# Optimization experiments

Measured on AMD Instinct MI355X. Metric: run time of the kernel, lower is better.

The kernel has to match this reference:

```python
import jax, jax.numpy as jnp
import numpy as np

Q_MAX = 127.0  # symmetric int8 range

def setup_inputs() -> dict:
    key = jax.random.key(0)
    k1, k2, k3, k4 = jax.random.split(key, 4)
    B, S, K, N = 4, 2048, 4096, 4096
    inp = jax.random.normal(k1, (B, S, K), dtype=jnp.float32)
    # int8 weight in [-127, 127], stored via randint(0,255)-127 per spec
    qweight = (jax.random.randint(k2, (N, K), 0, 255) - 127).astype(jnp.int8)
    # per-out-channel weight dequant scales (small positive)
    wparams = (jax.random.uniform(k3, (N,), dtype=jnp.float32) * 0.02 + 0.001)
    bias = jax.random.normal(k4, (N,), dtype=jnp.float32) * 0.1
    return {"inp": inp, "qweight": qweight, "wparams": wparams, "bias": bias}

def reference(inp, qweight, wparams, bias):
    # inp: [B, S, K] float32; qweight: [N, K] int8; wparams: [N]; bias: [N]
    B, S, K = inp.shape
    x = inp.reshape(B * S, K)
    # qntz: per-row symmetric absmax quantization of the activation to int8
    a_scale = jnp.max(jnp.abs(x), axis=1, keepdims=True) / Q_MAX  # [M, 1]
    qinp = jnp.clip(jnp.round(x / a_scale), -Q_MAX, Q_MAX).astype(jnp.int8)  # [M, K]
    d = jax.lax.dot_general(qinp, qweight.T, (((1,), (0,)), ((), ())),
                            preferred_element_type=jnp.int32)  # [M, N]
    # dqntz: scale by per-row act scale and per-col weight scale, add bias
    out = d.astype(jnp.float32) * a_scale * wparams[None, :] + bias[None, :]
    return out.reshape(B, S, -1)
```

## Files before the change

kernel.cpp:

```cpp
#include <hip/hip_runtime.h>
#include <hip/hip_bf16.h>


using int32x4 = __attribute__((ext_vector_type(4))) int;

#define QMAXF 127.0f

__global__ __launch_bounds__(256) void repack_weights(
    const int* __restrict__ w, signed char* __restrict__ w8, int total)
{
    bool is32 = true;
#pragma unroll
    for (int i = 0; i < 16; ++i) {
        int v = w[i];
        is32 = is32 && (v >= -127 && v <= 127);
    }

    const int t = blockIdx.x * blockDim.x + threadIdx.x;
    const int nth = gridDim.x * blockDim.x;
    const int chunks = total / 16;

    if (is32) {
        for (int c = t; c < chunks; c += nth) {
            const int32x4* src = reinterpret_cast<const int32x4*>(w + (size_t)c * 16);
            int32x4 a0 = src[0], a1 = src[1], a2 = src[2], a3 = src[3];
            int32x4 o;
            o[0] = (a0[0] & 0xff) | ((a0[1] & 0xff) << 8) | ((a0[2] & 0xff) << 16) | ((a0[3] & 0xff) << 24);
            o[1] = (a1[0] & 0xff) | ((a1[1] & 0xff) << 8) | ((a1[2] & 0xff) << 16) | ((a1[3] & 0xff) << 24);
            o[2] = (a2[0] & 0xff) | ((a2[1] & 0xff) << 8) | ((a2[2] & 0xff) << 16) | ((a2[3] & 0xff) << 24);
            o[3] = (a3[0] & 0xff) | ((a3[1] & 0xff) << 8) | ((a3[2] & 0xff) << 16) | ((a3[3] & 0xff) << 24);
            reinterpret_cast<int32x4*>(w8)[c] = o;
        }
    } else {
        const int32x4* src = reinterpret_cast<const int32x4*>(w);
        int32x4* dst = reinterpret_cast<int32x4*>(w8);
        for (int c = t; c < chunks; c += nth) dst[c] = src[c];
    }
}

__global__ __launch_bounds__(256) void quant_rows(
    const float* __restrict__ x, signed char* __restrict__ q,
    float* __restrict__ scale, int K)
{
    const int row = blockIdx.x;
    const int t = threadIdx.x;
    const float4* xr = reinterpret_cast<const float4*>(x + (size_t)row * K);

    float4 v[4];
    float m = 0.f;
#pragma unroll
    for (int i = 0; i < 4; ++i) {
        v[i] = xr[t + i * 256];
        m = fmaxf(m, fmaxf(fmaxf(fabsf(v[i].x), fabsf(v[i].y)),
                           fmaxf(fabsf(v[i].z), fabsf(v[i].w))));
    }
#pragma unroll
    for (int off = 32; off >= 1; off >>= 1)
        m = fmaxf(m, __shfl_xor(m, off, 64));
    __shared__ float wmax[4];
    const int wave = t >> 6;
    if ((t & 63) == 0) wmax[wave] = m;
    __syncthreads();
    m = fmaxf(fmaxf(wmax[0], wmax[1]), fmaxf(wmax[2], wmax[3]));

    const float s   = m / QMAXF;
    const float inv = (m > 0.f) ? (QMAXF / m) : 0.f;
    if (t == 0) scale[row] = s;

    int* qr = reinterpret_cast<int*>(q + (size_t)row * K);
#pragma unroll
    for (int i = 0; i < 4; ++i) {
        const float* f = reinterpret_cast<const float*>(&v[i]);
        unsigned int packed = 0;
#pragma unroll
        for (int j = 0; j < 4; ++j) {
            int qi = __float2int_rn(f[j] * inv);
            qi = qi > 127 ? 127 : (qi < -127 ? -127 : qi);
            packed |= ((unsigned int)(qi & 0xff)) << (8 * j);
        }
        qr[t + i * 256] = (int)packed;
    }
}

#define BM 256
#define BN 256
#define BKB 128

__device__ __forceinline__ void async_copy16(const void* g, void* lds) {
    __builtin_amdgcn_global_load_lds(
        (const __attribute__((address_space(1))) void*)g,
        (__attribute__((address_space(3))) void*)lds, 16, 0, 0);
}

__global__ __launch_bounds__(512, 2) void gemm_i8_dequant_256(
    const signed char* __restrict__ A,
    const signed char* __restrict__ B,
    const float* __restrict__ a_scale,
    const float* __restrict__ wparams,
    const float* __restrict__ bias,
    float* __restrict__ out,
    int M, int N, int K)
{
    __shared__ __align__(16) signed char lds[2 * 65536];

    const int t    = threadIdx.x;
    const int lane = t & 63;
    const int wave = t >> 6;
    const int wr   = wave >> 2;
    const int wc   = wave & 3;

    const int nwg = gridDim.x;
    const int cpx = nwg >> 3;
    const int swz = (blockIdx.x & 7) * cpx + (blockIdx.x >> 3);
    const int nbx = N / BN;
    const int rowBase = (swz / nbx) * BM;
    const int colBase = (swz % nbx) * BN;

    const int r15 = lane & 15;
    const int ksl = lane >> 4;

    int32x4 acc[8][4] = {};

    const int NT = K / BKB;

    auto stage = [&](int kt, int d) {
        signed char* base = lds + d * 65536;
#pragma unroll
        for (int j = 0; j < 4; ++j) {
            const int fi = j * 8 + wave;
            const int rg = fi >> 1, sl = fi & 1;
            const size_t coff = (size_t)kt + sl * 64 + ksl * 16;
            const signed char* gA = A + (size_t)(rowBase + rg * 16 + r15) * K + coff;
            const signed char* gB = B + (size_t)(colBase + rg * 16 + r15) * K + coff;
            async_copy16(gA, base + fi * 1024);
            async_copy16(gB, base + 32768 + fi * 1024);
        }
    };

    auto compute = [&](int d) {
        const signed char* Ab = lds + d * 65536;
        const signed char* Bb = Ab + 32768;
#pragma unroll
        for (int sl = 0; sl < 2; ++sl) {
            int32x4 af[8], bf[4];
#pragma unroll
            for (int mm = 0; mm < 8; ++mm)
                af[mm] = *reinterpret_cast<const int32x4*>(
                    Ab + ((wr * 8 + mm) * 2 + sl) * 1024 + lane * 16);
#pragma unroll
            for (int nn = 0; nn < 4; ++nn)
                bf[nn] = *reinterpret_cast<const int32x4*>(
                    Bb + ((wc * 4 + nn) * 2 + sl) * 1024 + lane * 16);
            __builtin_amdgcn_s_setprio(1);
#pragma unroll
            for (int mm = 0; mm < 8; ++mm)
#pragma unroll
                for (int nn = 0; nn < 4; ++nn)
                    acc[mm][nn] = __builtin_amdgcn_mfma_i32_16x16x64_i8(
                        af[mm], bf[nn], acc[mm][nn], 0, 0, 0);
            __builtin_amdgcn_s_setprio(0);
        }
    };

    stage(0, 0);
    __syncthreads();
    int cur = 0;
    for (int tt = 0; tt < NT - 1; ++tt) {
        stage((tt + 1) * BKB, cur ^ 1);
        compute(cur);
        __syncthreads();
        cur ^= 1;
    }
    compute(cur);

#pragma unroll
    for (int mm = 0; mm < 8; ++mm) {
        const int rb = rowBase + wr * 128 + mm * 16 + ksl * 4;
        float asc[4];
#pragma unroll
        for (int r = 0; r < 4; ++r) asc[r] = a_scale[rb + r];
#pragma unroll
        for (int nn = 0; nn < 4; ++nn) {
            const int col = colBase + wc * 64 + nn * 16 + r15;
            const float wp = wparams[col];
            const float bs = bias[col];
#pragma unroll
            for (int r = 0; r < 4; ++r) {
                out[(size_t)(rb + r) * N + col] =
                    (float)acc[mm][nn][r] * asc[r] * wp + bs;
            }
        }
    }
}

extern "C" void kernel_launch(void* const* d_in, const int* in_sizes, int n_in,
                              void* d_out, int out_size, void* d_ws, size_t ws_size,
                              hipStream_t stream) {
    const float* inp     = (const float*)d_in[0];
    const int*   qw_raw  = (const int*)d_in[1];
    const float* wparams = (const float*)d_in[2];
    const float* bias    = (const float*)d_in[3];
    float*       out     = (float*)d_out;

    const int N = in_sizes[2];
    const int K = in_sizes[1] / N;
    const int M = in_sizes[0] / K;

    signed char* qinp    = (signed char*)d_ws;
    float*       a_scale = (float*)((char*)d_ws + (size_t)M * K);
    size_t off_w8 = (size_t)M * K + (((size_t)M * sizeof(float) + 255) & ~(size_t)255);
    signed char* w8      = (signed char*)((char*)d_ws + off_w8);

    repack_weights<<<2048, 256, 0, stream>>>(qw_raw, w8, N * K);
    quant_rows<<<M, 256, 0, stream>>>(inp, qinp, a_scale, K);

    const int nwg = (M / BM) * (N / BN);
    gemm_i8_dequant_256<<<nwg, 512, 0, stream>>>(
        qinp, w8, a_scale, wparams, bias, out, M, N, K);
}
```

Baseline: 213.9 us.

## Use 4-stage LDS pipeline with BK=64 and interleaved staging in GEMM

The int8 GEMM's double-buffered K=128 tiles become a 4-deep ring of K=64 tiles. Each iteration issues the next A and B async global-to-LDS loads in two halves, interleaved between MFMA groups. A manual vmcnt wait keeps up to two tiles of loads in flight past each barrier, so global latency is hidden more deeply. The price is twice as many barriers per K, less MFMA work per barrier, and correctness that depends on the hand-counted vmcnt values.

```diff
diff --git a/kernel.cpp b/kernel.cpp
--- a/kernel.cpp
+++ b/kernel.cpp
@@ -84,7 +84,8 @@
 
 #define BM 256
 #define BN 256
-#define BKB 128
+#define BKB 64
+#define NBUF 4
 
 __device__ __forceinline__ void async_copy16(const void* g, void* lds) {
     __builtin_amdgcn_global_load_lds(
@@ -92,7 +93,7 @@
         (__attribute__((address_space(3))) void*)lds, 16, 0, 0);
 }
 
-__global__ __launch_bounds__(512, 2) void gemm_i8_dequant_256(
+__global__ __launch_bounds__(512, 2) void gemm_i8_dequant_8ph(
     const signed char* __restrict__ A,
     const signed char* __restrict__ B,
     const float* __restrict__ a_scale,
@@ -101,7 +102,7 @@
     float* __restrict__ out,
     int M, int N, int K)
 {
-    __shared__ __align__(16) signed char lds[2 * 65536];
+    __shared__ __align__(16) signed char lds[NBUF * 32768];
 
     const int t    = threadIdx.x;
     const int lane = t & 63;
@@ -120,58 +121,81 @@
     const int ksl = lane >> 4;
 
     int32x4 acc[8][4] = {};
-
     const int NT = K / BKB;
 
-    auto stage = [&](int kt, int d) {
-        signed char* base = lds + d * 65536;
-#pragma unroll
-        for (int j = 0; j < 4; ++j) {
-            const int fi = j * 8 + wave;
-            const int rg = fi >> 1, sl = fi & 1;
-            const size_t coff = (size_t)kt + sl * 64 + ksl * 16;
-            const signed char* gA = A + (size_t)(rowBase + rg * 16 + r15) * K + coff;
-            const signed char* gB = B + (size_t)(colBase + rg * 16 + r15) * K + coff;
-            async_copy16(gA, base + fi * 1024);
-            async_copy16(gB, base + 32768 + fi * 1024);
-        }
+    const signed char* gA0 = A + (size_t)(rowBase + wave * 16 + r15)       * K + ksl * 16;
+    const signed char* gA1 = A + (size_t)(rowBase + (8 + wave) * 16 + r15) * K + ksl * 16;
+    const signed char* gB0 = B + (size_t)(colBase + wave * 16 + r15)       * K + ksl * 16;
+    const signed char* gB1 = B + (size_t)(colBase + (8 + wave) * 16 + r15) * K + ksl * 16;
+
+    auto stageA = [&](int kt, int d) {
+        signed char* L = lds + d * 32768;
+        async_copy16(gA0 + kt, L + wave * 1024);
+        async_copy16(gA1 + kt, L + (8 + wave) * 1024);
     };
-
-    auto compute = [&](int d) {
-        const signed char* Ab = lds + d * 65536;
-        const signed char* Bb = Ab + 32768;
-#pragma unroll
-        for (int sl = 0; sl < 2; ++sl) {
-            int32x4 af[8], bf[4];
-#pragma unroll
-            for (int mm = 0; mm < 8; ++mm)
-                af[mm] = *reinterpret_cast<const int32x4*>(
-                    Ab + ((wr * 8 + mm) * 2 + sl) * 1024 + lane * 16);
+    auto stageB = [&](int kt, int d) {
+        signed char* L = lds + d * 32768 + 16384;
+        async_copy16(gB0 + kt, L + wave * 1024);
+        async_copy16(gB1 + kt, L + (8 + wave) * 1024);
+    };
+
+    auto computeTile = [&](int d, int tn, bool doStage) {
+        const signed char* Ab = lds + d * 32768;
+        const signed char* Bb = Ab + 16384;
+        const int dn = tn & (NBUF - 1);
+
+        if (doStage) stageA(tn * BKB, dn);
+        int32x4 af[8], bf[4];
+#pragma unroll
+        for (int mm = 0; mm < 4; ++mm)
+            af[mm] = *reinterpret_cast<const int32x4*>(
+                Ab + (wr * 8 + mm) * 1024 + lane * 16);
+#pragma unroll
+        for (int nn = 0; nn < 4; ++nn)
+            bf[nn] = *reinterpret_cast<const int32x4*>(
+                Bb + (wc * 4 + nn) * 1024 + lane * 16);
+        __builtin_amdgcn_s_setprio(1);
+#pragma unroll
+        for (int mm = 0; mm < 4; ++mm)
 #pragma unroll
             for (int nn = 0; nn < 4; ++nn)
-                bf[nn] = *reinterpret_cast<const int32x4*>(
-                    Bb + ((wc * 4 + nn) * 2 + sl) * 1024 + lane * 16);
-            __builtin_amdgcn_s_setprio(1);
-#pragma unroll
-            for (int mm = 0; mm < 8; ++mm)
-#pragma unroll
-                for (int nn = 0; nn < 4; ++nn)
-                    acc[mm][nn] = __builtin_amdgcn_mfma_i32_16x16x64_i8(
-                        af[mm], bf[nn], acc[mm][nn], 0, 0, 0);
-            __builtin_amdgcn_s_setprio(0);
-        }
+                acc[mm][nn] = __builtin_amdgcn_mfma_i32_16x16x64_i8(
+                    af[mm], bf[nn], acc[mm][nn], 0, 0, 0);
+        __builtin_amdgcn_s_setprio(0);
+
+        if (doStage) stageB(tn * BKB, dn);
+#pragma unroll
+        for (int mm = 4; mm < 8; ++mm)
+            af[mm] = *reinterpret_cast<const int32x4*>(
+                Ab + (wr * 8 + mm) * 1024 + lane * 16);
+        __builtin_amdgcn_s_setprio(1);
+#pragma unroll
+        for (int mm = 4; mm < 8; ++mm)
+#pragma unroll
+            for (int nn = 0; nn < 4; ++nn)
+                acc[mm][nn] = __builtin_amdgcn_mfma_i32_16x16x64_i8(
+                    af[mm], bf[nn], acc[mm][nn], 0, 0, 0);
+        __builtin_amdgcn_s_setprio(0);
     };
 
-    stage(0, 0);
-    __syncthreads();
-    int cur = 0;
-    for (int tt = 0; tt < NT - 1; ++tt) {
-        stage((tt + 1) * BKB, cur ^ 1);
-        compute(cur);
-        __syncthreads();
-        cur ^= 1;
-    }
-    compute(cur);
+    stageA(0, 0);        stageB(0, 0);
+    stageA(BKB, 1);      stageB(BKB, 1);
+    stageA(2 * BKB, 2);  stageB(2 * BKB, 2);
+    asm volatile("s_waitcnt vmcnt(8)" ::: "memory");
+    __builtin_amdgcn_s_barrier();
+
+    for (int tt = 0; tt <= NT - 4; ++tt) {
+        computeTile(tt & (NBUF - 1), tt + 3, true);
+        asm volatile("s_waitcnt vmcnt(8)" ::: "memory");
+        __builtin_amdgcn_s_barrier();
+    }
+    computeTile((NT - 3) & (NBUF - 1), 0, false);
+    asm volatile("s_waitcnt vmcnt(4)" ::: "memory");
+    __builtin_amdgcn_s_barrier();
+    computeTile((NT - 2) & (NBUF - 1), 0, false);
+    asm volatile("s_waitcnt vmcnt(0)" ::: "memory");
+    __builtin_amdgcn_s_barrier();
+    computeTile((NT - 1) & (NBUF - 1), 0, false);
 
 #pragma unroll
     for (int mm = 0; mm < 8; ++mm) {
@@ -215,6 +239,6 @@
     quant_rows<<<M, 256, 0, stream>>>(inp, qinp, a_scale, K);
 
     const int nwg = (M / BM) * (N / BN);
-    gemm_i8_dequant_256<<<nwg, 512, 0, stream>>>(
+    gemm_i8_dequant_8ph<<<nwg, 512, 0, stream>>>(
         qinp, w8, a_scale, wparams, bias, out, M, N, K);
 }
```

Result: faster. 203.4 us (-4.9%).

## Use four-stage LDS pipeline with split-phase MFMA and explicit waitcnts

Applied to the files above, without the earlier changes.

Replaces the double-buffered 128-byte K tile with a four-buffer pipeline of 64-byte K tiles, keeping three tiles in flight. Each iteration is split into two phases that interleave global-to-LDS async copies with LDS fragment loads and half of the MFMA work, using explicit s_waitcnt vmcnt and raw barriers in place of __syncthreads. The aim is to hide global load latency better and overlap memory traffic with matrix instructions. In exchange it issues four barriers per tile and relies on hand-tuned wait counts, which are fragile if the compiler reorders loads. LDS use stays at 128 KB.

```diff
diff --git a/kernel.cpp b/kernel.cpp
--- a/kernel.cpp
+++ b/kernel.cpp
@@ -84,7 +84,8 @@
 
 #define BM 256
 #define BN 256
-#define BKB 128
+#define BKB 64
+#define NBUF 4
 
 __device__ __forceinline__ void async_copy16(const void* g, void* lds) {
     __builtin_amdgcn_global_load_lds(
@@ -92,7 +93,69 @@
         (__attribute__((address_space(3))) void*)lds, 16, 0, 0);
 }
 
-__global__ __launch_bounds__(512, 2) void gemm_i8_dequant_256(
+#define BAR do {                                          \
+    __builtin_amdgcn_sched_barrier(0);                    \
+    asm volatile("" ::: "memory");                        \
+    __builtin_amdgcn_s_barrier();                         \
+    asm volatile("" ::: "memory");                        \
+    __builtin_amdgcn_sched_barrier(0);                    \
+} while (0)
+
+#define LGKM0 asm volatile("s_waitcnt lgkmcnt(0)" ::: "memory")
+#define VM8   asm volatile("s_waitcnt vmcnt(8)" ::: "memory")
+#define VM4   asm volatile("s_waitcnt vmcnt(4)" ::: "memory")
+#define VM0   asm volatile("s_waitcnt vmcnt(0)" ::: "memory")
+#define VMN   ((void)0)
+
+#define MFMA16(ACCB, AF, FB)                                                 \
+    __builtin_amdgcn_s_setprio(1);                                           \
+    _Pragma("unroll")                                                        \
+    for (int mm = 0; mm < 4; ++mm)                                           \
+        _Pragma("unroll")                                                    \
+        for (int nn = 0; nn < 4; ++nn)                                       \
+            acc[(ACCB) + mm][nn] = __builtin_amdgcn_mfma_i32_16x16x64_i8(    \
+                AF[mm], FB[nn], acc[(ACCB) + mm][nn], 0, 0, 0);              \
+    __builtin_amdgcn_s_setprio(0);
+
+#define TILE_ITER(T, DOSTAGE, VMASM)                                         \
+  {                                                                          \
+    const signed char* Ab = lds + ((T) & 3) * 32768 + wr * 8192 + lane * 16; \
+    const signed char* Bb = lds + ((T) & 3) * 32768 + 16384 + wc * 4096 + lane * 16; \
+    signed char* Ln = lds + (((T) + 3) & 3) * 32768;                         \
+    const size_t _kt = (size_t)((T) + 3) * BKB;                              \
+    int32x4 fb[4], af[4];                                                    \
+       \
+    fb[0] = *(const int32x4*)(Bb);                                           \
+    fb[1] = *(const int32x4*)(Bb + 1024);                                    \
+    fb[2] = *(const int32x4*)(Bb + 2048);                                    \
+    fb[3] = *(const int32x4*)(Bb + 3072);                                    \
+    af[0] = *(const int32x4*)(Ab);                                           \
+    af[1] = *(const int32x4*)(Ab + 1024);                                    \
+    af[2] = *(const int32x4*)(Ab + 2048);                                    \
+    af[3] = *(const int32x4*)(Ab + 3072);                                    \
+    if (DOSTAGE) {                                                           \
+        async_copy16(gA0 + _kt, Ln + wave * 1024);                           \
+        async_copy16(gA1 + _kt, Ln + (8 + wave) * 1024);                     \
+    }                                                                        \
+    BAR; LGKM0;                                                              \
+    MFMA16(0, af, fb);                                                       \
+    BAR;                                                                     \
+                 \
+    af[0] = *(const int32x4*)(Ab + 4096);                                    \
+    af[1] = *(const int32x4*)(Ab + 5120);                                    \
+    af[2] = *(const int32x4*)(Ab + 6144);                                    \
+    af[3] = *(const int32x4*)(Ab + 7168);                                    \
+    if (DOSTAGE) {                                                           \
+        async_copy16(gB0 + _kt, Ln + 16384 + wave * 1024);                   \
+        async_copy16(gB1 + _kt, Ln + 16384 + (8 + wave) * 1024);             \
+    }                                                                        \
+    VMASM;                                                                   \
+    BAR; LGKM0;                                                              \
+    MFMA16(4, af, fb);                                                       \
+    BAR;                                                                     \
+  }
+
+__global__ __launch_bounds__(512, 2) void gemm_i8_dequant_ph(
     const signed char* __restrict__ A,
     const signed char* __restrict__ B,
     const float* __restrict__ a_scale,
@@ -101,7 +164,7 @@
     float* __restrict__ out,
     int M, int N, int K)
 {
-    __shared__ __align__(16) signed char lds[2 * 65536];
+    __shared__ __align__(16) signed char lds[NBUF * 32768];
 
     const int t    = threadIdx.x;
     const int lane = t & 63;
@@ -120,58 +183,31 @@
     const int ksl = lane >> 4;
 
     int32x4 acc[8][4] = {};
-
     const int NT = K / BKB;
 
-    auto stage = [&](int kt, int d) {
-        signed char* base = lds + d * 65536;
-#pragma unroll
-        for (int j = 0; j < 4; ++j) {
-            const int fi = j * 8 + wave;
-            const int rg = fi >> 1, sl = fi & 1;
-            const size_t coff = (size_t)kt + sl * 64 + ksl * 16;
-            const signed char* gA = A + (size_t)(rowBase + rg * 16 + r15) * K + coff;
-            const signed char* gB = B + (size_t)(colBase + rg * 16 + r15) * K + coff;
-            async_copy16(gA, base + fi * 1024);
-            async_copy16(gB, base + 32768 + fi * 1024);
-        }
-    };
-
-    auto compute = [&](int d) {
-        const signed char* Ab = lds + d * 65536;
-        const signed char* Bb = Ab + 32768;
-#pragma unroll
-        for (int sl = 0; sl < 2; ++sl) {
-            int32x4 af[8], bf[4];
-#pragma unroll
-            for (int mm = 0; mm < 8; ++mm)
-                af[mm] = *reinterpret_cast<const int32x4*>(
-                    Ab + ((wr * 8 + mm) * 2 + sl) * 1024 + lane * 16);
-#pragma unroll
-            for (int nn = 0; nn < 4; ++nn)
-                bf[nn] = *reinterpret_cast<const int32x4*>(
-                    Bb + ((wc * 4 + nn) * 2 + sl) * 1024 + lane * 16);
-            __builtin_amdgcn_s_setprio(1);
-#pragma unroll
-            for (int mm = 0; mm < 8; ++mm)
-#pragma unroll
-                for (int nn = 0; nn < 4; ++nn)
-                    acc[mm][nn] = __builtin_amdgcn_mfma_i32_16x16x64_i8(
-                        af[mm], bf[nn], acc[mm][nn], 0, 0, 0);
-            __builtin_amdgcn_s_setprio(0);
-        }
-    };
-
-    stage(0, 0);
-    __syncthreads();
-    int cur = 0;
-    for (int tt = 0; tt < NT - 1; ++tt) {
-        stage((tt + 1) * BKB, cur ^ 1);
-        compute(cur);
-        __syncthreads();
-        cur ^= 1;
-    }
-    compute(cur);
+    const signed char* gA0 = A + (size_t)(rowBase + wave * 16 + r15)       * K + ksl * 16;
+    const signed char* gA1 = A + (size_t)(rowBase + (8 + wave) * 16 + r15) * K + ksl * 16;
+    const signed char* gB0 = B + (size_t)(colBase + wave * 16 + r15)       * K + ksl * 16;
+    const signed char* gB1 = B + (size_t)(colBase + (8 + wave) * 16 + r15) * K + ksl * 16;
+
+#pragma unroll
+    for (int p = 0; p < 3; ++p) {
+        signed char* L = lds + p * 32768;
+        const size_t kt = (size_t)p * BKB;
+        async_copy16(gA0 + kt, L + wave * 1024);
+        async_copy16(gA1 + kt, L + (8 + wave) * 1024);
+        async_copy16(gB0 + kt, L + 16384 + wave * 1024);
+        async_copy16(gB1 + kt, L + 16384 + (8 + wave) * 1024);
+    }
+    VM8;
+    BAR;
+
+    for (int tt = 0; tt < NT - 3; ++tt)
+        TILE_ITER(tt, true, VM8);
+
+    TILE_ITER(NT - 3, false, VM4);
+    TILE_ITER(NT - 2, false, VM0);
+    TILE_ITER(NT - 1, false, VMN);
 
 #pragma unroll
     for (int mm = 0; mm < 8; ++mm) {
@@ -215,6 +251,6 @@
     quant_rows<<<M, 256, 0, stream>>>(inp, qinp, a_scale, K);
 
     const int nwg = (M / BM) * (N / BN);
-    gemm_i8_dequant_256<<<nwg, 512, 0, stream>>>(
+    gemm_i8_dequant_ph<<<nwg, 512, 0, stream>>>(
         qinp, w8, a_scale, wparams, bias, out, M, N, K);
 }
```

Result: faster. 203.2 us (-5.0%).

## Triple-buffer 256x128 GEMM tiles with vmcnt waits and LDS-staged coalesced epilogue

Applied to the files above, without the earlier changes.

Tile shrinks from 256x256 with K-step 128 and 8 waves to 256x128 with K-step 64 and 4 waves. LDS becomes a three-stage ring with explicit s_waitcnt vmcnt plus raw barriers, so two tiles are in flight while one is computed. The epilogue writes dequantized results through LDS and emits coalesced float4 stores instead of scattered scalar stores. Smaller tiles raise the grid size and re-read A/B more, and the hand-counted vmcnt values must match the number of loads issued per stage.

```diff
diff --git a/kernel.cpp b/kernel.cpp
--- a/kernel.cpp
+++ b/kernel.cpp
@@ -83,8 +83,10 @@
 }
 
 #define BM 256
-#define BN 256
-#define BKB 128
+#define BN 128
+#define BKB 64
+#define NBUF 3
+#define BUFSZ 24576
 
 __device__ __forceinline__ void async_copy16(const void* g, void* lds) {
     __builtin_amdgcn_global_load_lds(
@@ -92,7 +94,18 @@
         (__attribute__((address_space(3))) void*)lds, 16, 0, 0);
 }
 
-__global__ __launch_bounds__(512, 2) void gemm_i8_dequant_256(
+#define BARF do {                                         \
+    __builtin_amdgcn_sched_barrier(0);                    \
+    asm volatile("" ::: "memory");                        \
+    __builtin_amdgcn_s_barrier();                         \
+    asm volatile("" ::: "memory");                        \
+    __builtin_amdgcn_sched_barrier(0);                    \
+} while (0)
+
+#define VM6   asm volatile("s_waitcnt vmcnt(6)" ::: "memory")
+#define VM0   asm volatile("s_waitcnt vmcnt(0)" ::: "memory")
+
+__global__ __launch_bounds__(256, 2) void gemm_i8_dequant_2b(
     const signed char* __restrict__ A,
     const signed char* __restrict__ B,
     const float* __restrict__ a_scale,
@@ -101,13 +114,13 @@
     float* __restrict__ out,
     int M, int N, int K)
 {
-    __shared__ __align__(16) signed char lds[2 * 65536];
+    __shared__ __align__(16) signed char lds[NBUF * BUFSZ];
 
     const int t    = threadIdx.x;
     const int lane = t & 63;
     const int wave = t >> 6;
-    const int wr   = wave >> 2;
-    const int wc   = wave & 3;
+    const int wr   = wave >> 1;
+    const int wc   = wave & 1;
 
     const int nwg = gridDim.x;
     const int cpx = nwg >> 3;
@@ -120,59 +133,72 @@
     const int ksl = lane >> 4;
 
     int32x4 acc[8][4] = {};
-
     const int NT = K / BKB;
 
-    auto stage = [&](int kt, int d) {
-        signed char* base = lds + d * 65536;
-#pragma unroll
-        for (int j = 0; j < 4; ++j) {
-            const int fi = j * 8 + wave;
-            const int rg = fi >> 1, sl = fi & 1;
-            const size_t coff = (size_t)kt + sl * 64 + ksl * 16;
-            const signed char* gA = A + (size_t)(rowBase + rg * 16 + r15) * K + coff;
-            const signed char* gB = B + (size_t)(colBase + rg * 16 + r15) * K + coff;
-            async_copy16(gA, base + fi * 1024);
-            async_copy16(gB, base + 32768 + fi * 1024);
-        }
+    const signed char* gA[4];
+#pragma unroll
+    for (int j = 0; j < 4; ++j)
+        gA[j] = A + (size_t)(rowBase + (j * 4 + wave) * 16 + r15) * K + ksl * 16;
+    const signed char* gB[2];
+#pragma unroll
+    for (int j = 0; j < 2; ++j)
+        gB[j] = B + (size_t)(colBase + (j * 4 + wave) * 16 + r15) * K + ksl * 16;
+
+    auto stage = [&](int tile, signed char* buf) {
+        const size_t kt = (size_t)tile * BKB;
+#pragma unroll
+        for (int j = 0; j < 4; ++j)
+            async_copy16(gA[j] + kt, buf + (j * 4 + wave) * 1024);
+#pragma unroll
+        for (int j = 0; j < 2; ++j)
+            async_copy16(gB[j] + kt, buf + 16384 + (j * 4 + wave) * 1024);
     };
 
-    auto compute = [&](int d) {
-        const signed char* Ab = lds + d * 65536;
-        const signed char* Bb = Ab + 32768;
-#pragma unroll
-        for (int sl = 0; sl < 2; ++sl) {
-            int32x4 af[8], bf[4];
-#pragma unroll
-            for (int mm = 0; mm < 8; ++mm)
-                af[mm] = *reinterpret_cast<const int32x4*>(
-                    Ab + ((wr * 8 + mm) * 2 + sl) * 1024 + lane * 16);
+    auto compute = [&](const signed char* buf) {
+        const signed char* Ab = buf + (wr * 8) * 1024 + lane * 16;
+        const signed char* Bb = buf + 16384 + (wc * 4) * 1024 + lane * 16;
+        int32x4 af[8], bf[4];
+#pragma unroll
+        for (int nn = 0; nn < 4; ++nn)
+            bf[nn] = *reinterpret_cast<const int32x4*>(Bb + nn * 1024);
+#pragma unroll
+        for (int mm = 0; mm < 8; ++mm)
+            af[mm] = *reinterpret_cast<const int32x4*>(Ab + mm * 1024);
+        __builtin_amdgcn_s_setprio(1);
+#pragma unroll
+        for (int mm = 0; mm < 8; ++mm)
 #pragma unroll
             for (int nn = 0; nn < 4; ++nn)
-                bf[nn] = *reinterpret_cast<const int32x4*>(
-                    Bb + ((wc * 4 + nn) * 2 + sl) * 1024 + lane * 16);
-            __builtin_amdgcn_s_setprio(1);
-#pragma unroll
-            for (int mm = 0; mm < 8; ++mm)
-#pragma unroll
-                for (int nn = 0; nn < 4; ++nn)
-                    acc[mm][nn] = __builtin_amdgcn_mfma_i32_16x16x64_i8(
-                        af[mm], bf[nn], acc[mm][nn], 0, 0, 0);
-            __builtin_amdgcn_s_setprio(0);
-        }
+                acc[mm][nn] = __builtin_amdgcn_mfma_i32_16x16x64_i8(
+                    af[mm], bf[nn], acc[mm][nn], 0, 0, 0);
+        __builtin_amdgcn_s_setprio(0);
     };
 
-    stage(0, 0);
-    __syncthreads();
-    int cur = 0;
-    for (int tt = 0; tt < NT - 1; ++tt) {
-        stage((tt + 1) * BKB, cur ^ 1);
-        compute(cur);
-        __syncthreads();
-        cur ^= 1;
-    }
-    compute(cur);
-
+    stage(0, lds);
+    stage(1, lds + BUFSZ);
+    VM6;
+    BARF;
+
+    int brd = 0;
+    for (int tt = 0; tt < NT - 2; ++tt) {
+        const int bw = brd == 0 ? 2 : brd - 1;
+        stage(tt + 2, lds + bw * BUFSZ);
+        compute(lds + brd * BUFSZ);
+        VM6;
+        BARF;
+        brd = brd == 2 ? 0 : brd + 1;
+    }
+    compute(lds + brd * BUFSZ);
+    VM0;
+    BARF;
+    brd = brd == 2 ? 0 : brd + 1;
+    compute(lds + brd * BUFSZ);
+    BARF;
+
+    signed char* ep = lds + wave * 4352;
+    const int col = colBase + wc * 64 + r15;
+    const float wp = wparams[col];
+    const float bs = bias[col];
 #pragma unroll
     for (int mm = 0; mm < 8; ++mm) {
         const int rb = rowBase + wr * 128 + mm * 16 + ksl * 4;
@@ -181,16 +207,26 @@
         for (int r = 0; r < 4; ++r) asc[r] = a_scale[rb + r];
 #pragma unroll
         for (int nn = 0; nn < 4; ++nn) {
-            const int col = colBase + wc * 64 + nn * 16 + r15;
-            const float wp = wparams[col];
-            const float bs = bias[col];
+            const float wpn = wparams[colBase + wc * 64 + nn * 16 + r15];
+            const float bsn = bias[colBase + wc * 64 + nn * 16 + r15];
 #pragma unroll
             for (int r = 0; r < 4; ++r) {
-                out[(size_t)(rb + r) * N + col] =
-                    (float)acc[mm][nn][r] * asc[r] * wp + bs;
+                const float v = (float)acc[mm][nn][r] * asc[r] * wpn + bsn;
+                *reinterpret_cast<float*>(
+                    ep + (ksl * 4 + r) * 272 + (nn * 16 + r15) * 4) = v;
             }
         }
-    }
+#pragma unroll
+        for (int it = 0; it < 4; ++it) {
+            const int row16 = it * 4 + ksl;
+            const float4 v = *reinterpret_cast<const float4*>(
+                ep + row16 * 272 + r15 * 16);
+            *reinterpret_cast<float4*>(
+                &out[(size_t)(rowBase + wr * 128 + mm * 16 + row16) * N +
+                     colBase + wc * 64 + r15 * 4]) = v;
+        }
+    }
+    (void)wp; (void)bs;
 }
 
 extern "C" void kernel_launch(void* const* d_in, const int* in_sizes, int n_in,
@@ -215,6 +251,6 @@
     quant_rows<<<M, 256, 0, stream>>>(inp, qinp, a_scale, K);
 
     const int nwg = (M / BM) * (N / BN);
-    gemm_i8_dequant_256<<<nwg, 512, 0, stream>>>(
+    gemm_i8_dequant_2b<<<nwg, 256, 0, stream>>>(
         qinp, w8, a_scale, wparams, bias, out, M, N, K);
 }
```

New measurement: 241.2 us. 12.8% more time.
